# Optimization experiments

Measured on AMD Instinct MI355X. Metric: run time of the kernel, lower is better.

Reference implementation:

```python
import jax, jax.numpy as jnp
import numpy as np

B, T, N, D, H = 16, 12, 325, 64, 4
E = 2600
NEG_SLOPE = 0.2
LN_EPS = 1e-5
SM_EPS = 1e-16


def setup_inputs() -> dict:
    key = jax.random.key(0)
    ks = jax.random.split(key, 8)
    x = jax.random.normal(ks[0], (B, T, N, D), dtype=jnp.float32)
    edge_index = jax.random.randint(ks[1], (2, E), 0, N, dtype=jnp.int64)
    W = jax.random.normal(ks[2], (D, H, D), dtype=jnp.float32) * 0.05   # lin weight, [in, heads, out]
    att_src = jax.random.normal(ks[3], (H, D), dtype=jnp.float32) * 0.05
    att_dst = jax.random.normal(ks[4], (H, D), dtype=jnp.float32) * 0.05
    bias = jnp.zeros((D,), dtype=jnp.float32)
    gamma = jnp.ones((D,), dtype=jnp.float32)
    beta = jnp.zeros((D,), dtype=jnp.float32)
    return {"x": x, "W": W, "att_src": att_src, "att_dst": att_dst,
            "bias": bias, "gamma": gamma, "beta": beta, "edge_index": edge_index}


def reference(x, W, att_src, att_dst, bias, gamma, beta, edge_index):
    b, t, n, d = x.shape
    bt = b * t
    xb = x.reshape(bt, n, d)

    # add self-loops (GATConv default add_self_loops=True)
    loops = jnp.arange(n, dtype=edge_index.dtype)
    src = jnp.concatenate([edge_index[0], loops])  # message source j
    dst = jnp.concatenate([edge_index[1], loops])  # message target i

    # per-head linear projection, node axis leading for segment ops: [N, BT, H, D]
    xp = jnp.einsum('bnd,dhf->nbhf', xb, W)

    a_src = jnp.einsum('nbhf,hf->nbh', xp, att_src)  # [N, BT, H]
    a_dst = jnp.einsum('nbhf,hf->nbh', xp, att_dst)

    alpha = a_src[src] + a_dst[dst]                  # [Etot, BT, H]
    alpha = jnp.where(alpha >= 0, alpha, NEG_SLOPE * alpha)

    # segment softmax over incoming edges of each dst node
    m = jax.ops.segment_max(alpha, dst, num_segments=n)        # [N, BT, H]
    e = jnp.exp(alpha - m[dst])
    s = jax.ops.segment_sum(e, dst, num_segments=n)            # [N, BT, H]
    coef = e / (s[dst] + SM_EPS)                               # [Etot, BT, H]

    # weighted scatter-sum aggregation
    msgs = coef[..., None] * xp[src]                           # [Etot, BT, H, D]
    out = jax.ops.segment_sum(msgs, dst, num_segments=n)       # [N, BT, H, D]

    out = out.mean(axis=2) + bias                              # concat=False -> head mean; [N, BT, D]
    out = out.transpose(1, 0, 2).reshape(b, t, n, d)

    # residual + LayerNorm
    y = x + out
    mu = y.mean(axis=-1, keepdims=True)
    var = y.var(axis=-1, keepdims=True)
    return (y - mu) * jax.lax.rsqrt(var + LN_EPS) * gamma + beta
```

## Files before the change

### kernel.cpp

```cpp
#include <hip/hip_runtime.h>

#define Nn 325
#define Dd 64
#define Hh 4
#define Ee 2600
#define BT 192
#define ETOT (Ee+Nn)
#define NROWS (BT*Nn)
#define XPS 136

typedef __attribute__((ext_vector_type(8))) short bf16x8;
typedef __attribute__((ext_vector_type(4))) float f32x4;

static __device__ __forceinline__ short f2bf(float f) {
    union { float f; unsigned u; } v; v.f = f;
    unsigned r = v.u + 0x7fffu + ((v.u >> 16) & 1u);
    return (short)(r >> 16);
}
static __device__ __forceinline__ float bf_lo(unsigned p) {
    union { unsigned u; float f; } v; v.u = p << 16; return v.f;
}
static __device__ __forceinline__ float bf_hi(unsigned p) {
    union { unsigned u; float f; } v; v.u = p & 0xffff0000u; return v.f;
}

__global__ __launch_bounds__(256) void k_pre(
    const float* __restrict__ W, unsigned short* __restrict__ Wt,
    const int* __restrict__ ei, int* __restrict__ offs, int* __restrict__ elist)
{
    const int t = threadIdx.x;
    if (blockIdx.x < 64) {
        const int f = blockIdx.x * 256 + t;
        const int thr = f >> 6, idx = f & 63;
        const int ct = idx >> 4, kk = (idx >> 3) & 1, j = idx & 7;
        const int w = thr >> 6, lane = thr & 63;
        const int q = lane >> 4, l16 = lane & 15;
        Wt[f] = (unsigned short)f2bf(
            W[(size_t)(kk * 32 + q * 8 + j) * 256 + w * 64 + ct * 16 + l16]);
        return;
    }
    __shared__ int cnt[Nn + 1];
    __shared__ int cur[Nn];
    const int lane = t & 63;
    for (int i = t; i <= Nn; i += 256) cnt[i] = 0;
    __syncthreads();
    for (int e = t; e < ETOT; e += 256) {
        int d = (e < Ee) ? ei[Ee + e] : (e - Ee);
        atomicAdd(&cnt[d + 1], 1);
    }
    __syncthreads();
    if (t < 64) {
        int run = 0;
        for (int c = 0; c < 6; ++c) {
            int i = c * 64 + lane;
            int v = (i <= Nn) ? cnt[i] : 0;
            #pragma unroll
            for (int off = 1; off < 64; off <<= 1) {
                int u = __shfl_up(v, off);
                if (lane >= off) v += u;
            }
            v += run;
            if (i <= Nn) cnt[i] = v;
            run = __shfl(v, 63);
        }
    }
    __syncthreads();
    for (int i = t; i <= Nn; i += 256) offs[i] = cnt[i];
    for (int i = t; i < Nn; i += 256) cur[i] = cnt[i];
    __syncthreads();
    for (int e = t; e < ETOT; e += 256) {
        int s, d;
        if (e < Ee) { s = ei[e]; d = ei[Ee + e]; }
        else        { s = e - Ee; d = e - Ee; }
        int slot = atomicAdd(&cur[d], 1);
        elist[slot] = s;
    }
}

__global__ __launch_bounds__(1024, 4) void k_fused(
    const float* __restrict__ x, const unsigned short* __restrict__ Wt,
    const float* __restrict__ att_src, const float* __restrict__ att_dst,
    const int* __restrict__ offs, const int* __restrict__ elist,
    const float* __restrict__ bias, const float* __restrict__ gamma,
    const float* __restrict__ beta, float* __restrict__ out)
{
    const int bt   = blockIdx.x;
    const int t    = threadIdx.x;
    const int wv   = t >> 6;
    const int lane = t & 63;
    const int q    = lane >> 4;
    const int l16  = lane & 15;
    const int btN  = bt * Nn;

    extern __shared__ char smem[];
    unsigned short* xpS   = (unsigned short*)smem;
    float*          asrcS = (float*)(smem + Nn * XPS * 2);
    float*          adstS = asrcS + 2 * Nn;
    int*            offsS = (int*)(adstS + 2 * Nn);
    int*            elistS= offsS + (Nn + 1);

    for (int i = t; i < ETOT; i += 1024) elistS[i] = elist[i];
    for (int i = t; i <= Nn; i += 1024) offsS[i] = offs[i];

    float accO[6][4];
    #pragma unroll
    for (int i = 0; i < 6; ++i)
        accO[i][0] = accO[i][1] = accO[i][2] = accO[i][3] = 0.f;

    const int hh  = wv >> 3;
    const int rtb = wv & 7;

    #pragma unroll 2
    for (int p = 0; p < 2; ++p) {
        const int h = p * 2 + hh;
        bf16x8 bfr[4][2];
        const bf16x8* wtp = (const bf16x8*)(Wt + (size_t)(h * 64 + lane) * 64);
        #pragma unroll
        for (int ct = 0; ct < 4; ++ct) {
            bfr[ct][0] = wtp[ct * 2];
            bfr[ct][1] = wtp[ct * 2 + 1];
        }
        float avs[4], avd[4];
        #pragma unroll
        for (int ct = 0; ct < 4; ++ct) {
            avs[ct] = att_src[h * 64 + ct * 16 + l16];
            avd[ct] = att_dst[h * 64 + ct * 16 + l16];
        }
        if (p) __syncthreads();

        #pragma unroll
        for (int k3 = 0; k3 < 3; ++k3) {
            const int rt = rtb + 8 * k3;
            if (rt > 20) break;
            bf16x8 afr[2];
            const int na = min(rt * 16 + l16, Nn - 1);
            const float* xr = x + (size_t)(btN + na) * 64 + q * 8;
            #pragma unroll
            for (int kk = 0; kk < 2; ++kk) {
                float4 v0 = *(const float4*)(xr + kk * 32);
                float4 v1 = *(const float4*)(xr + kk * 32 + 4);
                afr[kk][0]=f2bf(v0.x); afr[kk][1]=f2bf(v0.y);
                afr[kk][2]=f2bf(v0.z); afr[kk][3]=f2bf(v0.w);
                afr[kk][4]=f2bf(v1.x); afr[kk][5]=f2bf(v1.y);
                afr[kk][6]=f2bf(v1.z); afr[kk][7]=f2bf(v1.w);
            }
            f32x4 acc[4];
            #pragma unroll
            for (int ct = 0; ct < 4; ++ct) {
                acc[ct] = (f32x4){0.f, 0.f, 0.f, 0.f};
                acc[ct] = __builtin_amdgcn_mfma_f32_16x16x32_bf16(afr[0], bfr[ct][0], acc[ct], 0, 0, 0);
                acc[ct] = __builtin_amdgcn_mfma_f32_16x16x32_bf16(afr[1], bfr[ct][1], acc[ct], 0, 0, 0);
            }
            #pragma unroll
            for (int r = 0; r < 4; ++r) {
                const int n = rt * 16 + q * 4 + r;
                float ps = 0.f, pd = 0.f;
                #pragma unroll
                for (int ct = 0; ct < 4; ++ct) {
                    ps = fmaf(acc[ct][r], avs[ct], ps);
                    pd = fmaf(acc[ct][r], avd[ct], pd);
                }
                #pragma unroll
                for (int off = 1; off <= 8; off <<= 1) {
                    ps += __shfl_xor(ps, off);
                    pd += __shfl_xor(pd, off);
                }
                if (l16 == 0 && n < Nn) {
                    asrcS[n * 2 + hh] = ps;
                    adstS[n * 2 + hh] = pd;
                }
                if (n < Nn) {
                    #pragma unroll
                    for (int ct = 0; ct < 4; ++ct)
                        xpS[n * XPS + (ct * 16 + l16) * 2 + hh] =
                            (unsigned short)f2bf(acc[ct][r]);
                }
            }
        }
        __syncthreads();

        #pragma unroll
        for (int it = 0; it < 6; ++it) {
            const int n = wv * 4 + q + it * 64;
            if (n >= Nn) break;
            const int o0 = offsS[n];
            int deg = offsS[n + 1] - o0;
            deg = min(deg, 48);
            const float adn0 = adstS[n * 2], adn1 = adstS[n * 2 + 1];
            float ex0[3], ex1[3]; int jj[3];
            float m0 = -3e38f, m1 = -3e38f;
            #pragma unroll
            for (int r = 0; r < 3; ++r) {
                float a0 = -3e38f, a1 = -3e38f; int j = 0;
                if (r * 16 < deg) {
                    const int e = r * 16 + l16;
                    if (e < deg) {
                        j = elistS[o0 + e];
                        const float2 as = *(const float2*)(asrcS + j * 2);
                        a0 = as.x + adn0; a1 = as.y + adn1;
                    }
                }
                a0 = (a0 >= 0.f) ? a0 : 0.2f * a0;
                a1 = (a1 >= 0.f) ? a1 : 0.2f * a1;
                ex0[r] = a0; ex1[r] = a1; jj[r] = j;
                m0 = fmaxf(m0, a0); m1 = fmaxf(m1, a1);
            }
            #pragma unroll
            for (int off = 1; off <= 8; off <<= 1) {
                m0 = fmaxf(m0, __shfl_xor(m0, off));
                m1 = fmaxf(m1, __shfl_xor(m1, off));
            }
            float s0 = 0.f, s1 = 0.f;
            #pragma unroll
            for (int r = 0; r < 3; ++r) if (r * 16 < deg) {
                ex0[r] = __expf(ex0[r] - m0); s0 += ex0[r];
                ex1[r] = __expf(ex1[r] - m1); s1 += ex1[r];
            }
            #pragma unroll
            for (int off = 1; off <= 8; off <<= 1) {
                s0 += __shfl_xor(s0, off);
                s1 += __shfl_xor(s1, off);
            }
            const float i0 = 1.f / (s0 + 1e-16f);
            const float i1 = 1.f / (s1 + 1e-16f);
            #pragma unroll
            for (int r = 0; r < 3; ++r) { ex0[r] *= i0; ex1[r] *= i1; }

            float f0 = 0.f, f1 = 0.f, f2v = 0.f, f3 = 0.f;
            #pragma unroll
            for (int r = 0; r < 3; ++r) if (r * 16 < deg) {
                const int lim = min(16, deg - r * 16);
                for (int e2 = 0; e2 < lim; ++e2) {
                    const int src = q * 16 + e2;
                    const int jb  = __shfl(jj[r], src);
                    const float c0 = __shfl(ex0[r], src);
                    const float c1 = __shfl(ex1[r], src);
                    const uint4 rw = *(const uint4*)((const char*)xpS + jb * (XPS * 2) + l16 * 16);
                    f0 = fmaf(c0, bf_lo(rw.x), f0); f0 = fmaf(c1, bf_hi(rw.x), f0);
                    f1 = fmaf(c0, bf_lo(rw.y), f1); f1 = fmaf(c1, bf_hi(rw.y), f1);
                    f2v = fmaf(c0, bf_lo(rw.z), f2v); f2v = fmaf(c1, bf_hi(rw.z), f2v);
                    f3 = fmaf(c0, bf_lo(rw.w), f3); f3 = fmaf(c1, bf_hi(rw.w), f3);
                }
            }
            accO[it][0] += f0; accO[it][1] += f1;
            accO[it][2] += f2v; accO[it][3] += f3;
        }
    }

    const int f4 = l16 * 4;
    const float4 ga = *(const float4*)(gamma + f4);
    const float4 be = *(const float4*)(beta + f4);
    const float4 bi = *(const float4*)(bias + f4);
    #pragma unroll
    for (int it = 0; it < 6; ++it) {
        const int n = wv * 4 + q + it * 64;
        if (n >= Nn) break;
        const float4 xv = *(const float4*)(x + (size_t)(btN + n) * 64 + f4);
        const float y0 = xv.x + accO[it][0] * 0.25f + bi.x;
        const float y1 = xv.y + accO[it][1] * 0.25f + bi.y;
        const float y2 = xv.z + accO[it][2] * 0.25f + bi.z;
        const float y3 = xv.w + accO[it][3] * 0.25f + bi.w;
        float s1 = y0 + y1 + y2 + y3;
        float s2 = y0*y0 + y1*y1 + y2*y2 + y3*y3;
        #pragma unroll
        for (int off = 1; off <= 8; off <<= 1) {
            s1 += __shfl_xor(s1, off);
            s2 += __shfl_xor(s2, off);
        }
        const float mu  = s1 * (1.f / 64.f);
        const float var = s2 * (1.f / 64.f) - mu * mu;
        const float rr  = rsqrtf(var + 1e-5f);
        float4 o;
        o.x = (y0 - mu) * rr * ga.x + be.x;
        o.y = (y1 - mu) * rr * ga.y + be.y;
        o.z = (y2 - mu) * rr * ga.z + be.z;
        o.w = (y3 - mu) * rr * ga.w + be.w;
        *(float4*)(out + (size_t)(btN + n) * 64 + f4) = o;
    }
}

#define SMEM_BYTES (Nn * XPS * 2 + 2600 + 2600 + ((Nn + 1) * 4) + (ETOT * 4))

extern "C" void kernel_launch(void* const* d_in, const int* in_sizes, int n_in,
                              void* d_out, int out_size, void* d_ws, size_t ws_size,
                              hipStream_t stream)
{
    const float* x       = (const float*)d_in[0];
    const float* W       = (const float*)d_in[1];
    const float* att_src = (const float*)d_in[2];
    const float* att_dst = (const float*)d_in[3];
    const float* bias    = (const float*)d_in[4];
    const float* gamma   = (const float*)d_in[5];
    const float* beta    = (const float*)d_in[6];
    const int*   ei      = (const int*)d_in[7];

    unsigned short* Wt = (unsigned short*)d_ws;
    int* offs  = (int*)(Wt + 16384);
    int* elist = offs + (Nn + 1);
    float* out = (float*)d_out;

    hipFuncSetAttribute((const void*)k_fused,
                        hipFuncAttributeMaxDynamicSharedMemorySize, SMEM_BYTES);

    hipLaunchKernelGGL(k_pre, dim3(65), dim3(256), 0, stream,
                       W, Wt, ei, offs, elist);
    hipLaunchKernelGGL(k_fused, dim3(BT), dim3(1024), SMEM_BYTES, stream,
                       x, Wt, att_src, att_dst, offs, elist,
                       bias, gamma, beta, out);
}
```

Before: 144.3 us.

## Split each batch slice across two blocks, precast x to bf16, cache edge coefficients

The fused kernel now launches two 512-thread blocks per batch-time slice. Each block handles half of the destination nodes and walks all four heads one at a time, instead of two heads per pass. The pre-pass kernel converts x to bf16 in a workspace, so the fused kernel loads MFMA operands directly. Normalized softmax coefficients are stored next to the edge source index in shared memory, so aggregation reads them without cross-lane shuffles. Each block still recomputes the projection for all nodes (duplicated across the pair), and the extra conversion pass costs an additional read and write of x.

```diff
diff --git a/kernel.cpp b/kernel.cpp
--- a/kernel.cpp
+++ b/kernel.cpp
@@ -7,7 +7,12 @@
 #define BT 192
 #define ETOT (Ee+Nn)
 #define NROWS (BT*Nn)
-#define XPS 136
+#define XPS 68
+#define NH0 163
+
+#define XP_B (Nn * XPS * 2)
+#define EC_B (ETOT * 8)
+#define SMEM_BYTES (XP_B + EC_B + Nn*4 + Nn*4 + (Nn+1)*4)
 
 typedef __attribute__((ext_vector_type(8))) short bf16x8;
 typedef __attribute__((ext_vector_type(4))) float f32x4;
@@ -26,7 +31,8 @@
 
 __global__ __launch_bounds__(256) void k_pre(
     const float* __restrict__ W, unsigned short* __restrict__ Wt,
-    const int* __restrict__ ei, int* __restrict__ offs, int* __restrict__ elist)
+    const int* __restrict__ ei, int* __restrict__ offs, int* __restrict__ elist,
+    const float* __restrict__ x, unsigned short* __restrict__ xbf)
 {
     const int t = threadIdx.x;
     if (blockIdx.x < 64) {
@@ -39,6 +45,23 @@
             W[(size_t)(kk * 32 + q * 8 + j) * 256 + w * 64 + ct * 16 + l16]);
         return;
     }
+    if (blockIdx.x >= 65) {
+        const int bx = blockIdx.x - 65;
+        #pragma unroll
+        for (int k = 0; k < 8; ++k) {
+            const int idx = bx * 2048 + k * 256 + t;
+            if (idx < (NROWS * Dd) / 4) {
+                float4 v = ((const float4*)x)[idx];
+                ushort4 o;
+                o.x = (unsigned short)f2bf(v.x);
+                o.y = (unsigned short)f2bf(v.y);
+                o.z = (unsigned short)f2bf(v.z);
+                o.w = (unsigned short)f2bf(v.w);
+                ((ushort4*)xbf)[idx] = o;
+            }
+        }
+        return;
+    }
     __shared__ int cnt[Nn + 1];
     __shared__ int cur[Nn];
     const int lane = t & 63;
@@ -77,14 +100,16 @@
     }
 }
 
-__global__ __launch_bounds__(1024, 4) void k_fused(
-    const float* __restrict__ x, const unsigned short* __restrict__ Wt,
+__global__ __launch_bounds__(512, 4) void k_fused(
+    const unsigned short* __restrict__ xbf, const unsigned short* __restrict__ Wt,
+    const float* __restrict__ x,
     const float* __restrict__ att_src, const float* __restrict__ att_dst,
     const int* __restrict__ offs, const int* __restrict__ elist,
     const float* __restrict__ bias, const float* __restrict__ gamma,
     const float* __restrict__ beta, float* __restrict__ out)
 {
-    const int bt   = blockIdx.x;
+    const int bt   = blockIdx.x >> 1;
+    const int hf   = blockIdx.x & 1;
     const int t    = threadIdx.x;
     const int wv   = t >> 6;
     const int lane = t & 63;
@@ -94,27 +119,27 @@
 
     extern __shared__ char smem[];
     unsigned short* xpS   = (unsigned short*)smem;
-    float*          asrcS = (float*)(smem + Nn * XPS * 2);
-    float*          adstS = asrcS + 2 * Nn;
-    int*            offsS = (int*)(adstS + 2 * Nn);
-    int*            elistS= offsS + (Nn + 1);
-
-    for (int i = t; i < ETOT; i += 1024) elistS[i] = elist[i];
-    for (int i = t; i <= Nn; i += 1024) offsS[i] = offs[i];
+    int2*           ecS   = (int2*)(smem + XP_B);
+    float*          asrcS = (float*)(smem + XP_B + EC_B);
+    float*          adstS = asrcS + Nn;
+    int*            offsS = (int*)(adstS + Nn);
+
+    for (int i = t; i < ETOT; i += 512) ecS[i].x = elist[i];
+    for (int i = t; i <= Nn; i += 512) offsS[i] = offs[i];
+
+    const int nbase = hf ? NH0 : 0;
+    const int ncnt  = hf ? (Nn - NH0) : NH0;
+    const int g     = wv * 4 + q;
 
     float accO[6][4];
     #pragma unroll
     for (int i = 0; i < 6; ++i)
         accO[i][0] = accO[i][1] = accO[i][2] = accO[i][3] = 0.f;
 
-    const int hh  = wv >> 3;
-    const int rtb = wv & 7;
-
-    #pragma unroll 2
-    for (int p = 0; p < 2; ++p) {
-        const int h = p * 2 + hh;
+    #pragma unroll 1
+    for (int p = 0; p < 4; ++p) {
         bf16x8 bfr[4][2];
-        const bf16x8* wtp = (const bf16x8*)(Wt + (size_t)(h * 64 + lane) * 64);
+        const bf16x8* wtp = (const bf16x8*)(Wt + (size_t)(p * 64 + lane) * 64);
         #pragma unroll
         for (int ct = 0; ct < 4; ++ct) {
             bfr[ct][0] = wtp[ct * 2];
@@ -123,27 +148,20 @@
         float avs[4], avd[4];
         #pragma unroll
         for (int ct = 0; ct < 4; ++ct) {
-            avs[ct] = att_src[h * 64 + ct * 16 + l16];
-            avd[ct] = att_dst[h * 64 + ct * 16 + l16];
+            avs[ct] = att_src[p * 64 + ct * 16 + l16];
+            avd[ct] = att_dst[p * 64 + ct * 16 + l16];
         }
         if (p) __syncthreads();
 
         #pragma unroll
         for (int k3 = 0; k3 < 3; ++k3) {
-            const int rt = rtb + 8 * k3;
+            const int rt = wv + 8 * k3;
             if (rt > 20) break;
+            const int na = min(rt * 16 + l16, Nn - 1);
             bf16x8 afr[2];
-            const int na = min(rt * 16 + l16, Nn - 1);
-            const float* xr = x + (size_t)(btN + na) * 64 + q * 8;
-            #pragma unroll
-            for (int kk = 0; kk < 2; ++kk) {
-                float4 v0 = *(const float4*)(xr + kk * 32);
-                float4 v1 = *(const float4*)(xr + kk * 32 + 4);
-                afr[kk][0]=f2bf(v0.x); afr[kk][1]=f2bf(v0.y);
-                afr[kk][2]=f2bf(v0.z); afr[kk][3]=f2bf(v0.w);
-                afr[kk][4]=f2bf(v1.x); afr[kk][5]=f2bf(v1.y);
-                afr[kk][6]=f2bf(v1.z); afr[kk][7]=f2bf(v1.w);
-            }
+            #pragma unroll
+            for (int kk = 0; kk < 2; ++kk)
+                afr[kk] = *(const bf16x8*)(xbf + (size_t)(btN + na) * 64 + kk * 32 + q * 8);
             f32x4 acc[4];
             #pragma unroll
             for (int ct = 0; ct < 4; ++ct) {
@@ -165,82 +183,71 @@
                     ps += __shfl_xor(ps, off);
                     pd += __shfl_xor(pd, off);
                 }
-                if (l16 == 0 && n < Nn) {
-                    asrcS[n * 2 + hh] = ps;
-                    adstS[n * 2 + hh] = pd;
-                }
+                if (l16 == 0 && n < Nn) { asrcS[n] = ps; adstS[n] = pd; }
                 if (n < Nn) {
                     #pragma unroll
                     for (int ct = 0; ct < 4; ++ct)
-                        xpS[n * XPS + (ct * 16 + l16) * 2 + hh] =
-                            (unsigned short)f2bf(acc[ct][r]);
+                        xpS[n * XPS + ct * 16 + l16] = (unsigned short)f2bf(acc[ct][r]);
                 }
             }
         }
         __syncthreads();
 
-        #pragma unroll
+        #pragma unroll 1
         for (int it = 0; it < 6; ++it) {
-            const int n = wv * 4 + q + it * 64;
-            if (n >= Nn) break;
+            const int idx = it * 32 + g;
+            if (idx >= ncnt) break;
+            const int n = nbase + idx;
             const int o0 = offsS[n];
             int deg = offsS[n + 1] - o0;
             deg = min(deg, 48);
-            const float adn0 = adstS[n * 2], adn1 = adstS[n * 2 + 1];
-            float ex0[3], ex1[3]; int jj[3];
-            float m0 = -3e38f, m1 = -3e38f;
-            #pragma unroll
-            for (int r = 0; r < 3; ++r) {
-                float a0 = -3e38f, a1 = -3e38f; int j = 0;
-                if (r * 16 < deg) {
-                    const int e = r * 16 + l16;
-                    if (e < deg) {
-                        j = elistS[o0 + e];
-                        const float2 as = *(const float2*)(asrcS + j * 2);
-                        a0 = as.x + adn0; a1 = as.y + adn1;
-                    }
+            const float adn = adstS[n];
+
+            float ar[3];
+            float m = -3e38f;
+            #pragma unroll
+            for (int rr = 0; rr < 3; ++rr) {
+                if (rr * 16 >= deg) break;
+                const int e = rr * 16 + l16;
+                float a = -3e38f;
+                if (e < deg) {
+                    const int j = ecS[o0 + e].x;
+                    a = asrcS[j] + adn;
                 }
-                a0 = (a0 >= 0.f) ? a0 : 0.2f * a0;
-                a1 = (a1 >= 0.f) ? a1 : 0.2f * a1;
-                ex0[r] = a0; ex1[r] = a1; jj[r] = j;
-                m0 = fmaxf(m0, a0); m1 = fmaxf(m1, a1);
-            }
-            #pragma unroll
-            for (int off = 1; off <= 8; off <<= 1) {
-                m0 = fmaxf(m0, __shfl_xor(m0, off));
-                m1 = fmaxf(m1, __shfl_xor(m1, off));
-            }
-            float s0 = 0.f, s1 = 0.f;
-            #pragma unroll
-            for (int r = 0; r < 3; ++r) if (r * 16 < deg) {
-                ex0[r] = __expf(ex0[r] - m0); s0 += ex0[r];
-                ex1[r] = __expf(ex1[r] - m1); s1 += ex1[r];
-            }
-            #pragma unroll
-            for (int off = 1; off <= 8; off <<= 1) {
-                s0 += __shfl_xor(s0, off);
-                s1 += __shfl_xor(s1, off);
-            }
-            const float i0 = 1.f / (s0 + 1e-16f);
-            const float i1 = 1.f / (s1 + 1e-16f);
-            #pragma unroll
-            for (int r = 0; r < 3; ++r) { ex0[r] *= i0; ex1[r] *= i1; }
+                a = (a >= 0.f) ? a : 0.2f * a;
+                ar[rr] = a;
+                m = fmaxf(m, a);
+            }
+            #pragma unroll
+            for (int off = 1; off <= 8; off <<= 1) m = fmaxf(m, __shfl_xor(m, off));
+            float s = 0.f;
+            #pragma unroll
+            for (int rr = 0; rr < 3; ++rr) {
+                if (rr * 16 >= deg) break;
+                ar[rr] = __expf(ar[rr] - m);
+                s += ar[rr];
+            }
+            #pragma unroll
+            for (int off = 1; off <= 8; off <<= 1) s += __shfl_xor(s, off);
+            const float inv_s = 1.f / (s + 1e-16f);
+            #pragma unroll
+            for (int rr = 0; rr < 3; ++rr) {
+                if (rr * 16 >= deg) break;
+                const int e = rr * 16 + l16;
+                if (e < deg) ecS[o0 + e].y = __float_as_int(ar[rr] * inv_s);
+            }
 
             float f0 = 0.f, f1 = 0.f, f2v = 0.f, f3 = 0.f;
-            #pragma unroll
-            for (int r = 0; r < 3; ++r) if (r * 16 < deg) {
-                const int lim = min(16, deg - r * 16);
-                for (int e2 = 0; e2 < lim; ++e2) {
-                    const int src = q * 16 + e2;
-                    const int jb  = __shfl(jj[r], src);
-                    const float c0 = __shfl(ex0[r], src);
-                    const float c1 = __shfl(ex1[r], src);
-                    const uint4 rw = *(const uint4*)((const char*)xpS + jb * (XPS * 2) + l16 * 16);
-                    f0 = fmaf(c0, bf_lo(rw.x), f0); f0 = fmaf(c1, bf_hi(rw.x), f0);
-                    f1 = fmaf(c0, bf_lo(rw.y), f1); f1 = fmaf(c1, bf_hi(rw.y), f1);
-                    f2v = fmaf(c0, bf_lo(rw.z), f2v); f2v = fmaf(c1, bf_hi(rw.z), f2v);
-                    f3 = fmaf(c0, bf_lo(rw.w), f3); f3 = fmaf(c1, bf_hi(rw.w), f3);
-                }
+            #pragma unroll 4
+            for (int e2 = 0; e2 < deg; ++e2) {
+                const int2 ec = ecS[o0 + e2];
+                const float c = __int_as_float(ec.y);
+                const uint2 rw = *(const uint2*)((const char*)xpS +
+                                     ec.x * (XPS * 2) + l16 * 8);
+                f0  = fmaf(c, bf_lo(rw.x), f0);
+                f1  = fmaf(c, bf_hi(rw.x), f1);
+                f2v = fmaf(c, bf_lo(rw.y), f2v);
+                f3  = fmaf(c, bf_hi(rw.y), f3);
             }
             accO[it][0] += f0; accO[it][1] += f1;
             accO[it][2] += f2v; accO[it][3] += f3;
@@ -251,10 +258,11 @@
     const float4 ga = *(const float4*)(gamma + f4);
     const float4 be = *(const float4*)(beta + f4);
     const float4 bi = *(const float4*)(bias + f4);
-    #pragma unroll
+    #pragma unroll 1
     for (int it = 0; it < 6; ++it) {
-        const int n = wv * 4 + q + it * 64;
-        if (n >= Nn) break;
+        const int idx = it * 32 + g;
+        if (idx >= ncnt) break;
+        const int n = nbase + idx;
         const float4 xv = *(const float4*)(x + (size_t)(btN + n) * 64 + f4);
         const float y0 = xv.x + accO[it][0] * 0.25f + bi.x;
         const float y1 = xv.y + accO[it][1] * 0.25f + bi.y;
@@ -278,8 +286,6 @@
         *(float4*)(out + (size_t)(btN + n) * 64 + f4) = o;
     }
 }
-
-#define SMEM_BYTES (Nn * XPS * 2 + 2600 + 2600 + ((Nn + 1) * 4) + (ETOT * 4))
 
 extern "C" void kernel_launch(void* const* d_in, const int* in_sizes, int n_in,
                               void* d_out, int out_size, void* d_ws, size_t ws_size,
@@ -294,17 +300,18 @@
     const float* beta    = (const float*)d_in[6];
     const int*   ei      = (const int*)d_in[7];
 
-    unsigned short* Wt = (unsigned short*)d_ws;
-    int* offs  = (int*)(Wt + 16384);
+    unsigned short* Wt  = (unsigned short*)d_ws;
+    unsigned short* xbf = Wt + 16384;
+    int* offs  = (int*)(xbf + (size_t)NROWS * Dd);
     int* elist = offs + (Nn + 1);
     float* out = (float*)d_out;
 
     hipFuncSetAttribute((const void*)k_fused,
                         hipFuncAttributeMaxDynamicSharedMemorySize, SMEM_BYTES);
 
-    hipLaunchKernelGGL(k_pre, dim3(65), dim3(256), 0, stream,
-                       W, Wt, ei, offs, elist);
-    hipLaunchKernelGGL(k_fused, dim3(BT), dim3(1024), SMEM_BYTES, stream,
-                       x, Wt, att_src, att_dst, offs, elist,
+    hipLaunchKernelGGL(k_pre, dim3(65 + 488), dim3(256), 0, stream,
+                       W, Wt, ei, offs, elist, x, xbf);
+    hipLaunchKernelGGL(k_fused, dim3(2 * BT), dim3(512), SMEM_BYTES, stream,
+                       xbf, Wt, x, att_src, att_dst, offs, elist,
                        bias, gamma, beta, out);
 }
```

Measured after the change: 179.4 us. +24.3%, slower.
